# Performance work log

Measured on AMD Instinct MI355X. Metric: run time of the kernel, lower is better.

## Reference

```python
import jax, jax.numpy as jnp
import numpy as np

LOG2 = 0.6931471805599453  # shifted_softplus(x) = softplus(x) - log(2)
NUM_MOL = 20_000  # static maxm for segment reduction


def ssp(x):
    return jax.nn.softplus(x) - LOG2


def setup_inputs() -> dict:
    key = jax.random.key(0)
    ks = jax.random.split(key, 5)
    N, D, H, E, M = 1_000_000, 128, 64, 4, NUM_MOL
    x = jax.random.normal(ks[0], (N, D), dtype=jnp.float32)
    zidx = jax.random.randint(ks[1], (N,), 0, E, dtype=jnp.int32)
    idx_m = jnp.sort(jax.random.randint(ks[2], (N,), 0, M, dtype=jnp.int32))
    # stacked per-element pyramidal MLP params: D -> D//2 -> 1
    W1 = jax.random.normal(ks[3], (E, D, H), dtype=jnp.float32) * (1.0 / np.sqrt(D))
    b1 = jnp.zeros((E, H), dtype=jnp.float32)
    W2 = jax.random.normal(ks[4], (E, H, 1), dtype=jnp.float32) * (1.0 / np.sqrt(H))
    b2 = jnp.zeros((E, 1), dtype=jnp.float32)
    return dict(x=x, zidx=zidx, idx_m=idx_m, W1=W1, b1=b1, W2=W2, b2=b2)


def reference(x, zidx, idx_m, W1, b1, W2, b2):
    # ElementwiseMLP: run each element's 2-layer MLP, select per atom by element.
    E = W1.shape[0]
    yi = jnp.zeros((x.shape[0], W2.shape[-1]), dtype=x.dtype)  # [N, n_out]
    for e in range(E):  # small fixed element set
        h = ssp(x @ W1[e] + b1[e])            # [N, H]
        ye = h @ W2[e] + b2[e]                # [N, n_out]
        yi = yi + jnp.where((zidx == e)[:, None], ye, jnp.zeros((), dtype=x.dtype))
    # aggregation_mode == 'sum': index_add per molecule
    y = jax.ops.segment_sum(yi, idx_m, num_segments=NUM_MOL)  # [M, n_out]
    return jnp.squeeze(y, -1)  # [M]
```

## Files before the change

kernel.cpp:

```cpp
#include <hip/hip_runtime.h>

typedef _Float16 half8 __attribute__((ext_vector_type(8)));
typedef float f32x4 __attribute__((ext_vector_type(4)));

#define WS_COUNT(e)  ((e) * 32)
#define WS_CUR(e)    (160 + (e) * 32)
#define WS_PERM      512

__global__ void k_count(const int* __restrict__ zidx, int N, int* __restrict__ ws,
                        const float* __restrict__ W1, _Float16* __restrict__ w1h) {
  __shared__ int lh[4];
  if (threadIdx.x < 4) lh[threadIdx.x] = 0;
  if (blockIdx.x < 16) {
    const int cg = blockIdx.x * 256 + threadIdx.x;
    const int e = cg >> 10, ch = cg & 1023;
    const int kt = ch >> 8, nt = (ch >> 6) & 3, l2 = ch & 63;
    const int h = nt * 16 + (l2 & 15);
    const int d0 = kt * 32 + (l2 >> 4) * 8;
    const float* w1e = W1 + (size_t)e * 8192;
    half8 hv;
#pragma unroll
    for (int j = 0; j < 8; ++j) hv[j] = (_Float16)w1e[(d0 + j) * 64 + h];
    *(half8*)&w1h[(size_t)cg * 8] = hv;
  }
  __syncthreads();
  const int lane = threadIdx.x & 63;
  const int base = blockIdx.x * 1024;
  int pc[4] = {0, 0, 0, 0};
#pragma unroll
  for (int it = 0; it < 4; ++it) {
    const int i = base + it * 256 + threadIdx.x;
    const int z = (i < N) ? zidx[i] : -1;
#pragma unroll
    for (int e = 0; e < 4; ++e) {
      unsigned long long m = __ballot(z == e);
      if (lane == 0) pc[e] += __popcll(m);
    }
  }
  if (lane == 0) {
#pragma unroll
    for (int e = 0; e < 4; ++e)
      if (pc[e]) atomicAdd(&lh[e], pc[e]);
  }
  __syncthreads();
  if (threadIdx.x < 4 && lh[threadIdx.x])
    atomicAdd(&ws[WS_COUNT(threadIdx.x)], lh[threadIdx.x]);
}

__global__ void k_scatter(const int* __restrict__ zidx, int N, int* __restrict__ ws) {
  __shared__ int cnts[4][4][4];
  __shared__ int pb[4][4][4];
  const int tid = threadIdx.x, lane = tid & 63, wave = tid >> 6;
  const int base = blockIdx.x * 1024;
  int zz[4];
#pragma unroll
  for (int it = 0; it < 4; ++it) {
    const int i = base + it * 256 + tid;
    zz[it] = (i < N) ? zidx[i] : -1;
#pragma unroll
    for (int e = 0; e < 4; ++e) {
      unsigned long long m = __ballot(zz[it] == e);
      if (lane == 0) cnts[it][wave][e] = __popcll(m);
    }
  }
  __syncthreads();
  if (tid < 4) {
    const int e = tid;
    int off = 0, aoffe = 0;
#pragma unroll
    for (int k = 0; k < 4; ++k) {
      int ck = ws[WS_COUNT(k)];
      if (k == e) aoffe = off;
      off += (ck + 511) & ~511;
    }
    int tot = 0;
#pragma unroll
    for (int it = 0; it < 4; ++it)
#pragma unroll
      for (int w = 0; w < 4; ++w) tot += cnts[it][w][e];
    const int cur = atomicAdd(&ws[WS_CUR(e)], tot);
    int run = aoffe + cur;
#pragma unroll
    for (int it = 0; it < 4; ++it)
#pragma unroll
      for (int w = 0; w < 4; ++w) { pb[it][w][e] = run; run += cnts[it][w][e]; }
  }
  __syncthreads();
  const unsigned long long below = (1ull << lane) - 1ull;
#pragma unroll
  for (int it = 0; it < 4; ++it) {
    const int z = zz[it];
    const unsigned long long m0 = __ballot(z == 0);
    const unsigned long long m1 = __ballot(z == 1);
    const unsigned long long m2 = __ballot(z == 2);
    const unsigned long long m3 = __ballot(z == 3);
    if (z >= 0) {
      const unsigned long long me = (z == 0) ? m0 : (z == 1) ? m1 : (z == 2) ? m2 : m3;
      const int r = __popcll(me & below);
      ws[WS_PERM + pb[it][wave][z] + r] = base + it * 256 + tid;
    }
  }
}

#define LOADF(dst, g_) do {                                                     \
    const int ap_ = apv[g_];                                                    \
    const f32x4* rp_ = (const f32x4*)(x + (long)(ap_ < 0 ? 0 : ap_) * 128);     \
    _Pragma("unroll")                                                           \
    for (int kt = 0; kt < 4; ++kt) {                                            \
      f32x4 u0 = rp_[kt * 8 + q * 2];                                           \
      f32x4 u1 = rp_[kt * 8 + q * 2 + 1];                                       \
      half8 a;                                                                  \
      a[0] = (_Float16)u0[0]; a[1] = (_Float16)u0[1];                           \
      a[2] = (_Float16)u0[2]; a[3] = (_Float16)u0[3];                           \
      a[4] = (_Float16)u1[0]; a[5] = (_Float16)u1[1];                           \
      a[6] = (_Float16)u1[2]; a[7] = (_Float16)u1[3];                           \
      dst[kt] = a;                                                              \
    }                                                                           \
  } while (0)

#define COMPUTE(g_, af_) do {                                                   \
    f32x4 acc[4];                                                               \
    _Pragma("unroll")                                                           \
    for (int nt = 0; nt < 4; ++nt) acc[nt] = (f32x4){0.f, 0.f, 0.f, 0.f};       \
    _Pragma("unroll")                                                           \
    for (int kt = 0; kt < 4; ++kt)                                              \
      _Pragma("unroll")                                                         \
      for (int nt = 0; nt < 4; ++nt) {                                          \
        half8 bf = *(const half8*)&w1t[((kt * 4 + nt) * 64 + lane) * 8];        \
        acc[nt] = __builtin_amdgcn_mfma_f32_16x16x32_f16(af_[kt], bf, acc[nt], 0, 0, 0); \
      }                                                                         \
    float sv[4];                                                                \
    _Pragma("unroll")                                                           \
    for (int i = 0; i < 4; ++i) {                                               \
      float s = 0.0f;                                                           \
      _Pragma("unroll")                                                         \
      for (int nt = 0; nt < 4; ++nt) {                                          \
        float tv = acc[nt][i] + b1v[nt];                                        \
        float hsp = __logf(1.0f + __expf(tv)) - 0.69314718056f;                 \
        s = fmaf(hsp, w2v[nt], s);                                              \
      }                                                                         \
      s += __shfl_xor(s, 1);                                                    \
      s += __shfl_xor(s, 2);                                                    \
      s += __shfl_xor(s, 4);                                                    \
      s += __shfl_xor(s, 8);                                                    \
      sv[i] = s;                                                                \
    }                                                                           \
        \
    const int srcl = (lane >> 2) << 4;                                          \
    float t0 = __shfl(sv[0], srcl);                                             \
    float t1 = __shfl(sv[1], srcl);                                             \
    float t2 = __shfl(sv[2], srcl);                                             \
    float t3 = __shfl(sv[3], srcl);                                             \
    const int r3 = lane & 3;                                                    \
    float val = (r3 == 0) ? t0 : (r3 == 1) ? t1 : (r3 == 2) ? t2 : t3;          \
    const int apl = apv[g_];                                                    \
    const int ivl = ivv[g_];                                                    \
    val = (apl >= 0) ? val + b2e : 0.0f;                                        \
    const int ivp = __shfl_up(ivl, 1);                                          \
    const int head = (lane == 0) || (ivl != ivp);                               \
    int flg = head;                                                             \
    float v = val;                                                              \
    _Pragma("unroll")                                                           \
    for (int d = 1; d < 16; d <<= 1) {                                          \
      float v2 = __shfl_up(v, d);                                               \
      int f2 = __shfl_up(flg, d);                                               \
      if (lane >= d && !flg) v += v2;                                           \
      if (lane >= d) flg |= f2;                                                 \
    }                                                                           \
    const int nh = __shfl_down(head, 1);                                        \
    if (lane < 16 && ((lane == 15) || nh)) atomicAdd(&y[ivl], v);               \
  } while (0)

__global__ __launch_bounds__(256, 4)
void elemental_main(const float* __restrict__ x,
                    const int* __restrict__ idx_m,
                    const _Float16* __restrict__ w1h,
                    const float* __restrict__ b1,
                    const float* __restrict__ W2,
                    const float* __restrict__ b2,
                    const int* __restrict__ ws,
                    float* __restrict__ y) {
  __shared__ _Float16 w1t[8192];

  int cw[4];
#pragma unroll
  for (int k = 0; k < 4; ++k) cw[k] = ws[WS_COUNT(k)];
  const int aoff1 = (cw[0] + 511) & ~511;
  const int aoff2 = aoff1 + ((cw[1] + 511) & ~511);
  const int aoff3 = aoff2 + ((cw[2] + 511) & ~511);
  const int aoff4 = aoff3 + ((cw[3] + 511) & ~511);
  const int bstart = blockIdx.x * 512;
  if (bstart >= aoff4) return;
  int e = 0, ao = 0;
  if (bstart >= aoff1) { e = 1; ao = aoff1; }
  if (bstart >= aoff2) { e = 2; ao = aoff2; }
  if (bstart >= aoff3) { e = 3; ao = aoff3; }
  const int fillE = ao + cw[e];

  const int tid = threadIdx.x;
  const half8* src = (const half8*)w1h + (size_t)e * 1024;
#pragma unroll
  for (int it = 0; it < 4; ++it) {
    const int kk = it * 256 + tid;
    *(half8*)&w1t[kk * 8] = src[kk];
  }

  const int lane = tid & 63;
  const int wave = tid >> 6;
  const int c = lane & 15;
  const int q = lane >> 4;

  float b1v[4], w2v[4];
#pragma unroll
  for (int nt = 0; nt < 4; ++nt) {
    b1v[nt] = b1[e * 64 + nt * 16 + c];
    w2v[nt] = W2[e * 64 + nt * 16 + c];
  }
  const float b2e = b2[e];

  int apv[8], ivv[8];
  const int pbase = bstart + wave * 16 + c;
#pragma unroll
  for (int g = 0; g < 8; ++g) {
    const int pos = pbase + g * 64;
    apv[g] = (pos < fillE) ? ws[WS_PERM + pos] : -1;
  }
#pragma unroll
  for (int g = 0; g < 8; ++g)
    ivv[g] = (apv[g] >= 0) ? idx_m[apv[g]] : 0;

  __syncthreads();

  half8 afA[4], afB[4];
  LOADF(afA, 0);
  LOADF(afB, 1);
  COMPUTE(0, afA);
  LOADF(afA, 2);
  COMPUTE(1, afB);
  LOADF(afB, 3);
  COMPUTE(2, afA);
  LOADF(afA, 4);
  COMPUTE(3, afB);
  LOADF(afB, 5);
  COMPUTE(4, afA);
  LOADF(afA, 6);
  COMPUTE(5, afB);
  LOADF(afB, 7);
  COMPUTE(6, afA);
  COMPUTE(7, afB);
}

#define LDSROW_OLD 136

__global__ __launch_bounds__(256, 2)
void elemental_atomwise_kernel(const float* __restrict__ x,
                               const int* __restrict__ zidx,
                               const int* __restrict__ idx_m,
                               const float* __restrict__ W1,
                               const float* __restrict__ b1,
                               const float* __restrict__ W2,
                               const float* __restrict__ b2,
                               float* __restrict__ y,
                               int N) {
  extern __shared__ _Float16 w1t[];
#pragma unroll
  for (int it = 0; it < 32; ++it) {
    int idx4 = threadIdx.x + it * 256;
    f32x4 v = ((const f32x4*)W1)[idx4];
    int lin = idx4 << 2;
    int d = (lin >> 6) & 127;
    int ee = lin >> 13;
    int h = lin & 63;
    int n = ee * 64 + h;
#pragma unroll
    for (int j = 0; j < 4; ++j)
      w1t[(n + j) * LDSROW_OLD + d] = (_Float16)v[j];
  }
  __syncthreads();

  const int lane = threadIdx.x & 63;
  const int wave = threadIdx.x >> 6;
  const int c = lane & 15;
  const int q = lane >> 4;
  const long tile = (long)blockIdx.x * 4 + wave;
  const long base = tile * 64;
  if (base >= N) return;

  int ameta = (base + lane < N) ? (int)(base + lane) : (N - 1);
  const int zvec = zidx[ameta];
  const int ivec = idx_m[ameta];

  half8 af[4][4];
#pragma unroll
  for (int mt = 0; mt < 4; ++mt) {
    long row = base + mt * 16 + c;
    if (row >= N) row = N - 1;
    const f32x4* rp = (const f32x4*)(x + row * 128);
#pragma unroll
    for (int kt = 0; kt < 4; ++kt) {
      f32x4 u0 = rp[kt * 8 + q * 2];
      f32x4 u1 = rp[kt * 8 + q * 2 + 1];
      half8 a;
      a[0] = (_Float16)u0[0]; a[1] = (_Float16)u0[1];
      a[2] = (_Float16)u0[2]; a[3] = (_Float16)u0[3];
      a[4] = (_Float16)u1[0]; a[5] = (_Float16)u1[1];
      a[6] = (_Float16)u1[2]; a[7] = (_Float16)u1[3];
      af[mt][kt] = a;
    }
  }

#pragma unroll
  for (int e = 0; e < 4; ++e) {
    f32x4 acc[4][4];
#pragma unroll
    for (int mt = 0; mt < 4; ++mt)
#pragma unroll
      for (int nt = 0; nt < 4; ++nt)
        acc[mt][nt] = (f32x4){0.f, 0.f, 0.f, 0.f};

#pragma unroll
    for (int kt = 0; kt < 4; ++kt) {
#pragma unroll
      for (int nt = 0; nt < 4; ++nt) {
        half8 bf = *(const half8*)&w1t[(e * 64 + nt * 16 + c) * LDSROW_OLD + kt * 32 + q * 8];
#pragma unroll
        for (int mt = 0; mt < 4; ++mt)
          acc[mt][nt] = __builtin_amdgcn_mfma_f32_16x16x32_f16(af[mt][kt], bf, acc[mt][nt], 0, 0, 0);
      }
    }

    float b1v[4], w2v[4];
#pragma unroll
    for (int nt = 0; nt < 4; ++nt) {
      b1v[nt] = b1[e * 64 + nt * 16 + c];
      w2v[nt] = W2[e * 64 + nt * 16 + c];
    }
    const float b2e = b2[e];
#pragma unroll
    for (int mt = 0; mt < 4; ++mt) {
#pragma unroll
      for (int i = 0; i < 4; ++i) {
        float s = 0.0f;
#pragma unroll
        for (int nt = 0; nt < 4; ++nt) {
          float tv = acc[mt][nt][i] + b1v[nt];
          float hsp = __logf(1.0f + __expf(tv)) - 0.69314718056f;
          s = fmaf(hsp, w2v[nt], s);
        }
        s += __shfl_xor(s, 1);
        s += __shfl_xor(s, 2);
        s += __shfl_xor(s, 4);
        s += __shfl_xor(s, 8);
        int mloc = mt * 16 + q * 4 + i;
        int zm = __shfl(zvec, mloc);
        int im = __shfl(ivec, mloc);
        if (c == 0 && zm == e && base + mloc < N)
          atomicAdd(&y[im], s + b2e);
      }
    }
  }
}

extern "C" void kernel_launch(void* const* d_in, const int* in_sizes, int n_in,
                              void* d_out, int out_size, void* d_ws, size_t ws_size,
                              hipStream_t stream) {
  const float* x = (const float*)d_in[0];
  const int* zidx = (const int*)d_in[1];
  const int* idx_m = (const int*)d_in[2];
  const float* W1 = (const float*)d_in[3];
  const float* b1 = (const float*)d_in[4];
  const float* W2 = (const float*)d_in[5];
  const float* b2 = (const float*)d_in[6];
  float* y = (float*)d_out;

  const int N = in_sizes[0] / 128;

  hipMemsetAsync(d_out, 0, (size_t)out_size * sizeof(float), stream);

  const int w1h_off = (512 + N + 2048 + 3) & ~3;
  const size_t ws_need = (size_t)w1h_off * sizeof(int) + 65536;
  if (ws_size >= ws_need) {
    int* ws = (int*)d_ws;
    _Float16* w1h = (_Float16*)(ws + w1h_off);
    hipMemsetAsync(d_ws, 0, 2048, stream);
    const int nb = (N + 1023) / 1024;
    const int nbc = nb < 16 ? 16 : nb;
    k_count<<<nbc, 256, 0, stream>>>(zidx, N, ws, W1, w1h);
    k_scatter<<<nb, 256, 0, stream>>>(zidx, N, ws);
    const int mb = (N + 2555) / 512;
    elemental_main<<<mb, 256, 0, stream>>>(x, idx_m, w1h, b1, W2, b2, ws, y);
  } else {
    const int tiles = (N + 63) / 64;
    const int blocks = (tiles + 3) / 4;
    const size_t lds_bytes = 256 * LDSROW_OLD * sizeof(_Float16);
    elemental_atomwise_kernel<<<blocks, 256, lds_bytes, stream>>>(
        x, zidx, idx_m, W1, b1, W2, b2, y, N);
  }
}
```

Before: 703.9 us.

## Merge count into scatter with per-element buckets and loop-pipelined main kernel

```diff
diff --git a/kernel.cpp b/kernel.cpp
--- a/kernel.cpp
+++ b/kernel.cpp
@@ -3,14 +3,12 @@
 typedef _Float16 half8 __attribute__((ext_vector_type(8)));
 typedef float f32x4 __attribute__((ext_vector_type(4)));
 
-#define WS_COUNT(e)  ((e) * 32)
 #define WS_CUR(e)    (160 + (e) * 32)
 #define WS_PERM      512
 
-__global__ void k_count(const int* __restrict__ zidx, int N, int* __restrict__ ws,
-                        const float* __restrict__ W1, _Float16* __restrict__ w1h) {
-  __shared__ int lh[4];
-  if (threadIdx.x < 4) lh[threadIdx.x] = 0;
+__global__ void k_scatter(const int* __restrict__ zidx, const int* __restrict__ idx_m,
+                          int N, int Nr, int* __restrict__ ws,
+                          const float* __restrict__ W1, _Float16* __restrict__ w1h) {
   if (blockIdx.x < 16) {
     const int cg = blockIdx.x * 256 + threadIdx.x;
     const int e = cg >> 10, ch = cg & 1023;
@@ -23,40 +21,16 @@
     for (int j = 0; j < 8; ++j) hv[j] = (_Float16)w1e[(d0 + j) * 64 + h];
     *(half8*)&w1h[(size_t)cg * 8] = hv;
   }
-  __syncthreads();
-  const int lane = threadIdx.x & 63;
-  const int base = blockIdx.x * 1024;
-  int pc[4] = {0, 0, 0, 0};
-#pragma unroll
-  for (int it = 0; it < 4; ++it) {
-    const int i = base + it * 256 + threadIdx.x;
-    const int z = (i < N) ? zidx[i] : -1;
-#pragma unroll
-    for (int e = 0; e < 4; ++e) {
-      unsigned long long m = __ballot(z == e);
-      if (lane == 0) pc[e] += __popcll(m);
-    }
-  }
-  if (lane == 0) {
-#pragma unroll
-    for (int e = 0; e < 4; ++e)
-      if (pc[e]) atomicAdd(&lh[e], pc[e]);
-  }
-  __syncthreads();
-  if (threadIdx.x < 4 && lh[threadIdx.x])
-    atomicAdd(&ws[WS_COUNT(threadIdx.x)], lh[threadIdx.x]);
-}
-
-__global__ void k_scatter(const int* __restrict__ zidx, int N, int* __restrict__ ws) {
   __shared__ int cnts[4][4][4];
   __shared__ int pb[4][4][4];
   const int tid = threadIdx.x, lane = tid & 63, wave = tid >> 6;
   const int base = blockIdx.x * 1024;
-  int zz[4];
+  int zz[4], iv[4];
 #pragma unroll
   for (int it = 0; it < 4; ++it) {
     const int i = base + it * 256 + tid;
     zz[it] = (i < N) ? zidx[i] : -1;
+    iv[it] = (i < N) ? idx_m[i] : 0;
 #pragma unroll
     for (int e = 0; e < 4; ++e) {
       unsigned long long m = __ballot(zz[it] == e);
@@ -66,20 +40,12 @@
   __syncthreads();
   if (tid < 4) {
     const int e = tid;
-    int off = 0, aoffe = 0;
-#pragma unroll
-    for (int k = 0; k < 4; ++k) {
-      int ck = ws[WS_COUNT(k)];
-      if (k == e) aoffe = off;
-      off += (ck + 511) & ~511;
-    }
     int tot = 0;
 #pragma unroll
     for (int it = 0; it < 4; ++it)
 #pragma unroll
       for (int w = 0; w < 4; ++w) tot += cnts[it][w][e];
-    const int cur = atomicAdd(&ws[WS_CUR(e)], tot);
-    int run = aoffe + cur;
+    int run = tot ? atomicAdd(&ws[WS_CUR(e)], tot) : 0;
 #pragma unroll
     for (int it = 0; it < 4; ++it)
 #pragma unroll
@@ -97,13 +63,21 @@
     if (z >= 0) {
       const unsigned long long me = (z == 0) ? m0 : (z == 1) ? m1 : (z == 2) ? m2 : m3;
       const int r = __popcll(me & below);
-      ws[WS_PERM + pb[it][wave][z] + r] = base + it * 256 + tid;
+      const int dst = WS_PERM + z * Nr + pb[it][wave][z] + r;
+      ws[dst] = base + it * 256 + tid;
+      ws[dst + 4 * Nr] = iv[it];
     }
   }
 }
 
-#define LOADF(dst, g_) do {                                                     \
-    const int ap_ = apv[g_];                                                    \
+#define PRE(g_, pv_, iv_) do {                                                  \
+    const int pos_ = bstart + (g_) * 64 + wave * 16 + c;                        \
+    if (pos_ < fillE) { pv_ = permE[pos_]; iv_ = idxsE[pos_]; }                 \
+    else { pv_ = -1; iv_ = 0; }                                                 \
+  } while (0)
+
+#define LOADF(dst, pv_) do {                                                    \
+    const int ap_ = (pv_);                                                      \
     const f32x4* rp_ = (const f32x4*)(x + (long)(ap_ < 0 ? 0 : ap_) * 128);     \
     _Pragma("unroll")                                                           \
     for (int kt = 0; kt < 4; ++kt) {                                            \
@@ -118,7 +92,7 @@
     }                                                                           \
   } while (0)
 
-#define COMPUTE(g_, af_) do {                                                   \
+#define COMPUTE(af_, apl_, ivl_) do {                                           \
     f32x4 acc[4];                                                               \
     _Pragma("unroll")                                                           \
     for (int nt = 0; nt < 4; ++nt) acc[nt] = (f32x4){0.f, 0.f, 0.f, 0.f};       \
@@ -145,7 +119,7 @@
       s += __shfl_xor(s, 8);                                                    \
       sv[i] = s;                                                                \
     }                                                                           \
-        \
+                                    \
     const int srcl = (lane >> 2) << 4;                                          \
     float t0 = __shfl(sv[0], srcl);                                             \
     float t1 = __shfl(sv[1], srcl);                                             \
@@ -153,11 +127,9 @@
     float t3 = __shfl(sv[3], srcl);                                             \
     const int r3 = lane & 3;                                                    \
     float val = (r3 == 0) ? t0 : (r3 == 1) ? t1 : (r3 == 2) ? t2 : t3;          \
-    const int apl = apv[g_];                                                    \
-    const int ivl = ivv[g_];                                                    \
-    val = (apl >= 0) ? val + b2e : 0.0f;                                        \
-    const int ivp = __shfl_up(ivl, 1);                                          \
-    const int head = (lane == 0) || (ivl != ivp);                               \
+    val = ((apl_) >= 0) ? val + b2e : 0.0f;                                     \
+    const int ivp = __shfl_up((ivl_), 1);                                       \
+    const int head = (lane == 0) || ((ivl_) != ivp);                            \
     int flg = head;                                                             \
     float v = val;                                                              \
     _Pragma("unroll")                                                           \
@@ -168,34 +140,27 @@
       if (lane >= d) flg |= f2;                                                 \
     }                                                                           \
     const int nh = __shfl_down(head, 1);                                        \
-    if (lane < 16 && ((lane == 15) || nh)) atomicAdd(&y[ivl], v);               \
+    if (lane < 16 && ((lane == 15) || nh)) atomicAdd(&y[(ivl_)], v);            \
   } while (0)
 
 __global__ __launch_bounds__(256, 4)
 void elemental_main(const float* __restrict__ x,
-                    const int* __restrict__ idx_m,
                     const _Float16* __restrict__ w1h,
                     const float* __restrict__ b1,
                     const float* __restrict__ W2,
                     const float* __restrict__ b2,
                     const int* __restrict__ ws,
-                    float* __restrict__ y) {
+                    float* __restrict__ y,
+                    int Nr, int bpe) {
   __shared__ _Float16 w1t[8192];
 
-  int cw[4];
-#pragma unroll
-  for (int k = 0; k < 4; ++k) cw[k] = ws[WS_COUNT(k)];
-  const int aoff1 = (cw[0] + 511) & ~511;
-  const int aoff2 = aoff1 + ((cw[1] + 511) & ~511);
-  const int aoff3 = aoff2 + ((cw[2] + 511) & ~511);
-  const int aoff4 = aoff3 + ((cw[3] + 511) & ~511);
-  const int bstart = blockIdx.x * 512;
-  if (bstart >= aoff4) return;
-  int e = 0, ao = 0;
-  if (bstart >= aoff1) { e = 1; ao = aoff1; }
-  if (bstart >= aoff2) { e = 2; ao = aoff2; }
-  if (bstart >= aoff3) { e = 3; ao = aoff3; }
-  const int fillE = ao + cw[e];
+  const int e = blockIdx.x / bpe;
+  const int bi = blockIdx.x - e * bpe;
+  const int fillE = ws[WS_CUR(e)];
+  const int bstart = bi << 10;
+  if (bstart >= fillE) return;
+  const int* permE = ws + WS_PERM + (size_t)e * Nr;
+  const int* idxsE = permE + 4 * (size_t)Nr;
 
   const int tid = threadIdx.x;
   const half8* src = (const half8*)w1h + (size_t)e * 1024;
@@ -218,36 +183,28 @@
   }
   const float b2e = b2[e];
 
-  int apv[8], ivv[8];
-  const int pbase = bstart + wave * 16 + c;
-#pragma unroll
-  for (int g = 0; g < 8; ++g) {
-    const int pos = pbase + g * 64;
-    apv[g] = (pos < fillE) ? ws[WS_PERM + pos] : -1;
-  }
-#pragma unroll
-  for (int g = 0; g < 8; ++g)
-    ivv[g] = (apv[g] >= 0) ? idx_m[apv[g]] : 0;
-
+  int pv0, iv0, pv1, iv1;
+  half8 af0[4], af1[4];
+  PRE(0, pv0, iv0);
+  PRE(1, pv1, iv1);
+  LOADF(af0, pv0);
   __syncthreads();
 
-  half8 afA[4], afB[4];
-  LOADF(afA, 0);
-  LOADF(afB, 1);
-  COMPUTE(0, afA);
-  LOADF(afA, 2);
-  COMPUTE(1, afB);
-  LOADF(afB, 3);
-  COMPUTE(2, afA);
-  LOADF(afA, 4);
-  COMPUTE(3, afB);
-  LOADF(afB, 5);
-  COMPUTE(4, afA);
-  LOADF(afA, 6);
-  COMPUTE(5, afB);
-  LOADF(afB, 7);
-  COMPUTE(6, afA);
-  COMPUTE(7, afB);
+#pragma unroll 1
+  for (int g = 0; g < 16; g += 2) {
+    LOADF(af1, pv1);
+    {
+      const int apl = pv0, ivl = iv0;
+      if (g + 2 < 16) PRE(g + 2, pv0, iv0);
+      COMPUTE(af0, apl, ivl);
+    }
+    if (g + 2 < 16) LOADF(af0, pv0);
+    {
+      const int apl = pv1, ivl = iv1;
+      if (g + 3 < 16) PRE(g + 3, pv1, iv1);
+      COMPUTE(af1, apl, ivl);
+    }
+  }
 }
 
 #define LDSROW_OLD 136
@@ -377,18 +334,17 @@
 
   hipMemsetAsync(d_out, 0, (size_t)out_size * sizeof(float), stream);
 
-  const int w1h_off = (512 + N + 2048 + 3) & ~3;
-  const size_t ws_need = (size_t)w1h_off * sizeof(int) + 65536;
+  const int bpe = (N + 1023) >> 10;
+  const int Nr = bpe << 10;
+  const size_t w1h_off = ((size_t)512 + 8 * (size_t)Nr + 3) & ~(size_t)3;
+  const size_t ws_need = w1h_off * sizeof(int) + 65536;
   if (ws_size >= ws_need) {
     int* ws = (int*)d_ws;
     _Float16* w1h = (_Float16*)(ws + w1h_off);
     hipMemsetAsync(d_ws, 0, 2048, stream);
-    const int nb = (N + 1023) / 1024;
-    const int nbc = nb < 16 ? 16 : nb;
-    k_count<<<nbc, 256, 0, stream>>>(zidx, N, ws, W1, w1h);
-    k_scatter<<<nb, 256, 0, stream>>>(zidx, N, ws);
-    const int mb = (N + 2555) / 512;
-    elemental_main<<<mb, 256, 0, stream>>>(x, idx_m, w1h, b1, W2, b2, ws, y);
+    const int nbs = bpe < 16 ? 16 : bpe;
+    k_scatter<<<nbs, 256, 0, stream>>>(zidx, idx_m, N, Nr, ws, W1, w1h);
+    elemental_main<<<4 * bpe, 256, 0, stream>>>(x, w1h, b1, W2, b2, ws, y, Nr, bpe);
   } else {
     const int tiles = (N + 63) / 64;
     const int blocks = (tiles + 3) / 4;
```

Measured after the change: 731.8 us. +4.0%, slower.
